# Kernel tuning notes

Hardware: AMD Instinct MI355X
Metric: run time of the kernel (lower is better)

The kernel has to match this reference:

```python
import jax, jax.numpy as jnp
import numpy as np

DIM = 1024
HID = 2816
N_ROUTED = 7  # num_experts - num_shared_experts
TOPK = 2
B, S = 4, 2048


def _expert(x, wg, wu, wd):
    # DeepSeekExpertLayer: down(silu(gate(x)) * up(x)); weights stored [in, out]
    return (jax.nn.silu(x @ wg) * (x @ wu)) @ wd


def setup_inputs() -> dict:
    key = jax.random.key(0)
    ks = jax.random.split(key, 9)
    s = 0.02
    x = jax.random.normal(ks[0], (B, S, DIM), jnp.float32)
    shared_gate = jax.random.normal(ks[1], (DIM, HID), jnp.float32) * s
    shared_up = jax.random.normal(ks[2], (DIM, HID), jnp.float32) * s
    shared_down = jax.random.normal(ks[3], (HID, DIM), jnp.float32) * s
    routed_gate = jax.random.normal(ks[4], (N_ROUTED, DIM, HID), jnp.float32) * s
    routed_up = jax.random.normal(ks[5], (N_ROUTED, DIM, HID), jnp.float32) * s
    routed_down = jax.random.normal(ks[6], (N_ROUTED, HID, DIM), jnp.float32) * s
    Wr = jax.random.normal(ks[7], (DIM, N_ROUTED), jnp.float32) * s
    # NOTE: original inits routing_bias to zeros (degenerate routing since logits
    # are MULTIPLIED by it); use random values so routing is non-trivial.
    routing_bias = jax.random.normal(ks[8], (N_ROUTED,), jnp.float32)
    return dict(x=x, shared_gate=shared_gate, shared_up=shared_up, shared_down=shared_down,
                routed_gate=routed_gate, routed_up=routed_up, routed_down=routed_down,
                Wr=Wr, routing_bias=routing_bias)


def reference(x, shared_gate, shared_up, shared_down,
              routed_gate, routed_up, routed_down, Wr, routing_bias):
    b, s, d = x.shape
    n_exp = routed_gate.shape[0]
    # shared expert path (num_shared_experts == 1, no division)
    shared_out = _expert(x, shared_gate, shared_up, shared_down)
    # router: note logits are MULTIPLIED by routing_bias (faithful to source)
    logits = (x @ Wr) * routing_bias            # [b, s, E]
    probs = jax.nn.sigmoid(logits)
    scores, idx = jax.lax.top_k(probs, TOPK)    # [b, s, k]
    scores = scores / scores.sum(-1, keepdims=True)
    # per-token per-expert combine weight via scatter-add of top-k scores
    t = b * s
    xf = x.reshape(t, d)
    weights = jnp.zeros((t, n_exp), x.dtype).at[
        jnp.arange(t)[:, None], idx.reshape(t, TOPK)].add(scores.reshape(t, TOPK))
    combined = jnp.zeros_like(xf)
    for e in range(n_exp):  # static small loop over experts
        combined = combined + _expert(xf, routed_gate[e], routed_up[e], routed_down[e]) * weights[:, e:e + 1]
    return shared_out + combined.reshape(b, s, d)
```

## Files before the change

### kernel.cpp

```cpp
#include <hip/hip_runtime.h>
#include <hip/hip_bf16.h>

#define DIM 1024
#define HID 2816
#define NEXP 7
#define TOKENS 8192
#define NT16 (DIM / 64)

#define MW3_XB    0ull
#define MW3_WGU   16777216ull
#define MW3_WD    109051904ull
#define MW3_H     155189248ull
#define MW3_TOK   303693824ull
#define MW3_WGT   303799296ull
#define MW3_SLT   303904768ull
#define MW3_META  303970304ull
#define MW3_NEED  303972352ull

#define MW_XB    0ull
#define MW_H     16777216ull
#define MW_WGU   114098176ull
#define MW_WD    206372864ull
#define MW_TOK   252510208ull
#define MW_WGT   252579328ull
#define MW_META  252648448ull
#define MW_NEED  252650496ull

typedef __bf16 bf16x8 __attribute__((ext_vector_type(8)));
typedef float f32x4 __attribute__((ext_vector_type(4)));

static __device__ __forceinline__ unsigned short f2b(float f) {
  union { float f; unsigned int i; } c; c.f = f;
  unsigned int i = c.i;
  unsigned int r = (i + 0x7fffu + ((i >> 16) & 1u)) >> 16;
  return (unsigned short)r;
}

static __device__ __forceinline__ void gload16(const void* g, void* l) {
  __builtin_amdgcn_global_load_lds(
      (const __attribute__((address_space(1))) unsigned int*)g,
      (__attribute__((address_space(3))) unsigned int*)l, 16, 0, 0);
}

__global__ __launch_bounds__(256, 2) void router_kernel(
    const float* __restrict__ X,
    const float* __restrict__ Wr,
    const float* __restrict__ bias,
    int* __restrict__ eidx,
    float* __restrict__ ew)
{
  __shared__ float wr[DIM * NEXP];
  for (int i = threadIdx.x; i < DIM * NEXP; i += 256) wr[i] = Wr[i];
  __syncthreads();
  int t = blockIdx.x * 256 + threadIdx.x;
  float acc[NEXP];
#pragma unroll
  for (int e = 0; e < NEXP; ++e) acc[e] = 0.f;
  const float* xp = X + (size_t)t * DIM;
  for (int d0 = 0; d0 < DIM; d0 += 4) {
    float4 xv = *(const float4*)(xp + d0);
    const float* xs = (const float*)&xv;
#pragma unroll
    for (int j = 0; j < 4; ++j) {
      float xf = xs[j];
#pragma unroll
      for (int e = 0; e < NEXP; ++e) acc[e] += xf * wr[(d0 + j) * NEXP + e];
    }
  }
  float p[NEXP];
#pragma unroll
  for (int e = 0; e < NEXP; ++e)
    p[e] = 1.f / (1.f + __expf(-acc[e] * bias[e]));
  float best = -1.f; int bi = 0;
#pragma unroll
  for (int e = 0; e < NEXP; ++e) if (p[e] > best) { best = p[e]; bi = e; }
  float sec = -1.f; int si = 0;
#pragma unroll
  for (int e = 0; e < NEXP; ++e) if (e != bi && p[e] > sec) { sec = p[e]; si = e; }
  float s = best + sec;
  eidx[t] = bi | (si << 8);
  ((float2*)ew)[t] = make_float2(best / s, sec / s);
}

__global__ __launch_bounds__(256) void xcvt_kernel(
    const float* __restrict__ X, unsigned short* __restrict__ Xb)
{
  int i = (blockIdx.x * 256 + threadIdx.x) * 8;
  float4 v0 = *(const float4*)&X[i];
  float4 v1 = *(const float4*)&X[i + 4];
  unsigned short o[8];
  o[0] = f2b(v0.x); o[1] = f2b(v0.y); o[2] = f2b(v0.z); o[3] = f2b(v0.w);
  o[4] = f2b(v1.x); o[5] = f2b(v1.y); o[6] = f2b(v1.z); o[7] = f2b(v1.w);
  *(int4*)&Xb[i] = *(const int4*)o;
}

__global__ __launch_bounds__(256) void build3_kernel(
    const int* __restrict__ eidx, const float* __restrict__ ew,
    int* __restrict__ tok, float* __restrict__ wgt,
    int2* __restrict__ slt, int* __restrict__ meta)
{
  __shared__ int cnt[NEXP], fill[NEXP], ofs[NEXP];
  const int tid = threadIdx.x;
  const int lane = tid & 63, wid = tid >> 6;
  if (tid < NEXP) { cnt[tid] = 0; fill[tid] = 0; }
  for (int i = tid; i < TOKENS; i += 256) { tok[i] = i; wgt[i] = 1.f; }
  __syncthreads();
  const unsigned long long lmask = (1ull << lane) - 1ull;
  for (int base = wid * 64; base < TOKENS; base += 256) {
    int t = base + lane;
    int p = eidx[t];
    int e0 = p & 0xff, e1 = (p >> 8) & 0xff;
#pragma unroll
    for (int e = 0; e < NEXP; ++e) {
      unsigned long long m0 = __ballot(e0 == e);
      unsigned long long m1 = __ballot(e1 == e);
      if (lane == 0) {
        int tot = __popcll(m0) + __popcll(m1);
        if (tot) atomicAdd(&cnt[e], tot);
      }
    }
  }
  __syncthreads();
  if (tid == 0) {
    int o = 0, nb = 0, nb2 = 0;
    meta[0] = TOKENS; meta[8] = 0;
    for (int i = 0; i < TOKENS / 256; ++i) meta[32 + nb++] = 0 | (i << 4);
    for (int i = 0; i < TOKENS / 128; ++i) meta[160 + nb2++] = 0 | (i << 4);
    for (int e = 0; e < NEXP; ++e) {
      ofs[e] = o;
      meta[1 + e] = cnt[e];
      meta[9 + e] = TOKENS + o;
      int b = (cnt[e] + 255) >> 8;
      for (int i = 0; i < b; ++i)     meta[32 + nb++]   = (e + 1) | (i << 4);
      for (int i = 0; i < 2 * b; ++i) meta[160 + nb2++] = (e + 1) | (i << 4);
      o += b << 8;
    }
    meta[16] = nb; meta[17] = nb2;
  }
  __syncthreads();
  for (int base = wid * 64; base < TOKENS; base += 256) {
    int t = base + lane;
    int p = eidx[t];
    int e0 = p & 0xff, e1 = (p >> 8) & 0xff;
    float2 w = ((const float2*)ew)[t];
    int s0 = 0, s1 = 0;
#pragma unroll
    for (int e = 0; e < NEXP; ++e) {
      unsigned long long m0 = __ballot(e0 == e);
      unsigned long long m1 = __ballot(e1 == e);
      int tot = __popcll(m0) + __popcll(m1);
      int wb = 0;
      if (lane == 0 && tot) wb = atomicAdd(&fill[e], tot);
      wb = __shfl(wb, 0);
      if (e0 == e) {
        int sl = TOKENS + ofs[e] + wb + __popcll(m0 & lmask);
        tok[sl] = t; wgt[sl] = w.x; s0 = sl;
      }
      if (e1 == e) {
        int sl = TOKENS + ofs[e] + wb + __popcll(m0) + __popcll(m1 & lmask);
        tok[sl] = t; wgt[sl] = w.y; s1 = sl;
      }
    }
    slt[t] = make_int2(s0, s1);
  }
}

__global__ __launch_bounds__(256) void transpose_all_kernel(
    const float* __restrict__ sg, const float* __restrict__ su, const float* __restrict__ sd,
    const float* __restrict__ rg, const float* __restrict__ ru, const float* __restrict__ rd,
    unsigned short* __restrict__ WguA, unsigned short* __restrict__ WdA)
{
  int b = blockIdx.x;
  int e = b / 2112, r = b % 2112;
  int m = r / 704, q2 = r % 704;
  const float* src; unsigned short* dst; int K, N, nb, kb;
  if (m == 0) {
    src = e ? rg + (size_t)(e - 1) * DIM * HID : sg;
    dst = WguA + (size_t)e * (2 * (size_t)HID * DIM);
    K = DIM; N = HID; nb = q2 % 44; kb = q2 / 44;
  } else if (m == 1) {
    src = e ? ru + (size_t)(e - 1) * DIM * HID : su;
    dst = WguA + (size_t)e * (2 * (size_t)HID * DIM) + (size_t)HID * DIM;
    K = DIM; N = HID; nb = q2 % 44; kb = q2 / 44;
  } else {
    src = e ? rd + (size_t)(e - 1) * HID * DIM : sd;
    dst = WdA + (size_t)e * ((size_t)HID * DIM);
    K = HID; N = DIM; nb = q2 % 16; kb = q2 / 16;
  }
  __shared__ unsigned short t[64][72];
  const int n0 = nb * 64, k0 = kb * 64;
  const int tid = threadIdx.x;
  const int kl = tid >> 4, nl = (tid & 15) * 4;
#pragma unroll
  for (int i = 0; i < 4; ++i) {
    int k = kl + i * 16;
    float4 v = *(const float4*)&src[(size_t)(k0 + k) * N + n0 + nl];
    t[nl + 0][k] = f2b(v.x); t[nl + 1][k] = f2b(v.y);
    t[nl + 2][k] = f2b(v.z); t[nl + 3][k] = f2b(v.w);
  }
  __syncthreads();
  const int nl2 = tid >> 3, kc = (tid & 7) * 8;
#pragma unroll
  for (int i = 0; i < 2; ++i) {
    int n = nl2 + i * 32;
    *(int4*)&dst[(size_t)(n0 + n) * K + k0 + kc] = *(const int4*)&t[n][kc];
  }
}

__global__ __launch_bounds__(512, 2) void gateup8_kernel(
    const unsigned short* __restrict__ Xb,
    const unsigned short* __restrict__ WguA,
    const int* __restrict__ tok, const float* __restrict__ wgt,
    const int* __restrict__ meta,
    unsigned short* __restrict__ H)
{
  const int yb = blockIdx.y;
  if (yb >= meta[16]) return;
  const int ent = meta[32 + yb];
  const int e = ent & 15, mb = ent >> 4;
  const int cnt = meta[e];
  const int pofs = meta[8 + e];
  const int m0 = mb * 256;
  const unsigned short* Wg = WguA + (size_t)e * (2 * (size_t)HID * DIM);
  const unsigned short* Wu = Wg + (size_t)HID * DIM;

  __shared__ __align__(16) unsigned short As[3][256 * 64];
  __shared__ __align__(16) unsigned short Bgs[3][64 * 64];
  __shared__ __align__(16) unsigned short Bus[3][64 * 64];
  __shared__ float wl[256];

  const int tid = threadIdx.x;
  const int lane = tid & 63;
  const int w = tid >> 6;
  const int wmi = w & 3;
  const int wni = w >> 2;
  const int c = lane & 15;
  const int q = lane >> 4;
  const int cx = c & 7;

  const int srow = tid >> 3;
  const int swz = ((tid & 7) ^ (srow & 7)) * 8;

  const unsigned short* aptr[4];
#pragma unroll
  for (int i = 0; i < 4; ++i) {
    int s = m0 + i * 64 + srow;
    int t = (s < cnt) ? tok[pofs + s] : 0;
    aptr[i] = Xb + (size_t)t * DIM + swz;
  }
  const int n0 = blockIdx.x * 64;
  const unsigned short* gptr = Wg + (size_t)(n0 + srow) * DIM + swz;
  const unsigned short* uptr = Wu + (size_t)(n0 + srow) * DIM + swz;

  if (tid < 256) wl[tid] = (m0 + tid < cnt) ? wgt[pofs + m0 + tid] : 0.f;

#pragma unroll
  for (int t = 0; t < 2; ++t) {
#pragma unroll
    for (int i = 0; i < 4; ++i) gload16(aptr[i] + t * 64, &As[t][i * 4096 + tid * 8]);
    gload16(gptr + t * 64, &Bgs[t][tid * 8]);
    gload16(uptr + t * 64, &Bus[t][tid * 8]);
  }
  __syncthreads();

  f32x4 accg[4][2], accu[4][2];
#pragma unroll
  for (int mi = 0; mi < 4; ++mi)
#pragma unroll
    for (int ni = 0; ni < 2; ++ni) {
      accg[mi][ni] = {0.f, 0.f, 0.f, 0.f};
      accu[mi][ni] = {0.f, 0.f, 0.f, 0.f};
    }

  int b = 0, bs = 2;
#pragma unroll 1
  for (int t = 0; t < NT16; ++t) {
    bf16x8 a[4][2], bg[2][2];
#pragma unroll
    for (int mi = 0; mi < 4; ++mi)
#pragma unroll
      for (int ks = 0; ks < 2; ++ks)
        a[mi][ks] = *(const bf16x8*)&As[b][(wmi * 64 + mi * 16 + c) * 64 + (((ks * 4 + q) ^ cx) * 8)];
#pragma unroll
    for (int ni = 0; ni < 2; ++ni)
#pragma unroll
      for (int ks = 0; ks < 2; ++ks)
        bg[ni][ks] = *(const bf16x8*)&Bgs[b][(wni * 32 + ni * 16 + c) * 64 + (((ks * 4 + q) ^ cx) * 8)];
    if (t + 2 < NT16) {
      const int k2 = (t + 2) * 64;
      gload16(aptr[0] + k2, &As[bs][0 * 4096 + tid * 8]);
      gload16(aptr[1] + k2, &As[bs][1 * 4096 + tid * 8]);
      gload16(aptr[2] + k2, &As[bs][2 * 4096 + tid * 8]);
    }
    __builtin_amdgcn_s_barrier();
    asm volatile("s_waitcnt lgkmcnt(0)" ::: "memory");
    __builtin_amdgcn_sched_barrier(0);
    __builtin_amdgcn_s_setprio(1);
#pragma unroll
    for (int mi = 0; mi < 4; ++mi)
#pragma unroll
      for (int ni = 0; ni < 2; ++ni) {
        accg[mi][ni] = __builtin_amdgcn_mfma_f32_16x16x32_bf16(a[mi][0], bg[ni][0], accg[mi][ni], 0, 0, 0);
        accg[mi][ni] = __builtin_amdgcn_mfma_f32_16x16x32_bf16(a[mi][1], bg[ni][1], accg[mi][ni], 0, 0, 0);
      }
    __builtin_amdgcn_s_setprio(0);
    __builtin_amdgcn_sched_barrier(0);
    __builtin_amdgcn_s_barrier();
    __builtin_amdgcn_sched_barrier(0);

    bf16x8 bu[2][2];
#pragma unroll
    for (int ni = 0; ni < 2; ++ni)
#pragma unroll
      for (int ks = 0; ks < 2; ++ks)
        bu[ni][ks] = *(const bf16x8*)&Bus[b][(wni * 32 + ni * 16 + c) * 64 + (((ks * 4 + q) ^ cx) * 8)];
    if (t + 2 < NT16) {
      const int k2 = (t + 2) * 64;
      gload16(aptr[3] + k2, &As[bs][3 * 4096 + tid * 8]);
      gload16(gptr + k2, &Bgs[bs][tid * 8]);
      gload16(uptr + k2, &Bus[bs][tid * 8]);
      asm volatile("s_waitcnt vmcnt(6)" ::: "memory");
    } else if (t + 1 < NT16) {
      asm volatile("s_waitcnt vmcnt(0)" ::: "memory");
    }
    __builtin_amdgcn_s_barrier();
    asm volatile("s_waitcnt lgkmcnt(0)" ::: "memory");
    __builtin_amdgcn_sched_barrier(0);
    __builtin_amdgcn_s_setprio(1);
#pragma unroll
    for (int mi = 0; mi < 4; ++mi)
#pragma unroll
      for (int ni = 0; ni < 2; ++ni) {
        accu[mi][ni] = __builtin_amdgcn_mfma_f32_16x16x32_bf16(a[mi][0], bu[ni][0], accu[mi][ni], 0, 0, 0);
        accu[mi][ni] = __builtin_amdgcn_mfma_f32_16x16x32_bf16(a[mi][1], bu[ni][1], accu[mi][ni], 0, 0, 0);
      }
    __builtin_amdgcn_s_setprio(0);
    __builtin_amdgcn_sched_barrier(0);
    __builtin_amdgcn_s_barrier();
    __builtin_amdgcn_sched_barrier(0);

    b = (b == 2) ? 0 : b + 1;
    bs = (bs == 2) ? 0 : bs + 1;
  }

#pragma unroll
  for (int mi = 0; mi < 4; ++mi)
#pragma unroll
    for (int ni = 0; ni < 2; ++ni)
#pragma unroll
      for (int r = 0; r < 4; ++r) {
        int row = wmi * 64 + mi * 16 + q * 4 + r;
        int col = wni * 32 + ni * 16 + c;
        float g = accg[mi][ni][r];
        float u = accu[mi][ni][r];
        float h = (g / (1.f + __expf(-g))) * u * wl[row];
        H[(size_t)(pofs + m0 + row) * HID + n0 + col] = f2b(h);
      }
}

__global__ __launch_bounds__(256, 2) void down_all_kernel(
    const unsigned short* __restrict__ Hm,
    const unsigned short* __restrict__ WdA,
    const int* __restrict__ meta,
    float* __restrict__ P)
{
  const int yb = blockIdx.y;
  if (yb >= meta[17]) return;
  const int ent = meta[160 + yb];
  const int e = ent & 15, mb = ent >> 4;
  const int pofs = meta[8 + e];
  const unsigned short* WdT = WdA + (size_t)e * ((size_t)HID * DIM);

  __shared__ __align__(16) unsigned short As[128 * 64];
  __shared__ __align__(16) unsigned short Bs[128 * 64];
  const int n0 = blockIdx.x * 128;
  const int tid = threadIdx.x;
  const int lane = tid & 63;
  const int w4 = tid >> 6;
  const int wm = (w4 & 1) * 64;
  const int wn = (w4 >> 1) * 64;
  const int c = lane & 15;
  const int q = lane >> 4;
  const int cx = c & 7;

  const int r8 = lane >> 3;
  const int swz = ((lane & 7) ^ r8) * 8;
  const int wrow = w4 * 8 + r8;

  const unsigned short* aptr[4];
  const unsigned short* bptr[4];
#pragma unroll
  for (int i = 0; i < 4; ++i) {
    aptr[i] = Hm + (size_t)(pofs + mb * 128 + i * 32 + wrow) * HID + swz;
    bptr[i] = WdT + (size_t)(n0 + i * 32 + wrow) * HID + swz;
  }

  f32x4 acc[4][4];
#pragma unroll
  for (int mi = 0; mi < 4; ++mi)
#pragma unroll
    for (int ni = 0; ni < 4; ++ni) acc[mi][ni] = {0.f, 0.f, 0.f, 0.f};

  for (int k0 = 0; k0 < HID; k0 += 64) {
    __syncthreads();
#pragma unroll
    for (int i = 0; i < 4; ++i) {
      gload16(aptr[i] + k0, &As[i * 2048 + tid * 8]);
      gload16(bptr[i] + k0, &Bs[i * 2048 + tid * 8]);
    }
    __syncthreads();
#pragma unroll
    for (int h = 0; h < 2; ++h) {
      const int go = ((h * 4 + q) ^ cx) * 8;
      bf16x8 a[4], bb[4];
#pragma unroll
      for (int mi = 0; mi < 4; ++mi)
        a[mi] = *(const bf16x8*)&As[(wm + mi * 16 + c) * 64 + go];
#pragma unroll
      for (int ni = 0; ni < 4; ++ni)
        bb[ni] = *(const bf16x8*)&Bs[(wn + ni * 16 + c) * 64 + go];
#pragma unroll
      for (int mi = 0; mi < 4; ++mi)
#pragma unroll
        for (int ni = 0; ni < 4; ++ni)
          acc[mi][ni] = __builtin_amdgcn_mfma_f32_16x16x32_bf16(a[mi], bb[ni], acc[mi][ni], 0, 0, 0);
    }
  }
#pragma unroll
  for (int mi = 0; mi < 4; ++mi)
#pragma unroll
    for (int r = 0; r < 4; ++r) {
      int prow = pofs + mb * 128 + wm + mi * 16 + q * 4 + r;
#pragma unroll
      for (int ni = 0; ni < 4; ++ni) {
        int col = n0 + wn + ni * 16 + c;
        P[(size_t)prow * DIM + col] = acc[mi][ni][r];
      }
    }
}

__global__ __launch_bounds__(256) void combine_kernel(
    const float* __restrict__ P, const int2* __restrict__ slt,
    float* __restrict__ out)
{
  const int t = blockIdx.x;
  const int2 s = slt[t];
  const int d = threadIdx.x;
  float4 a = ((const float4*)(P + (size_t)t * DIM))[d];
  float4 b = ((const float4*)(P + (size_t)s.x * DIM))[d];
  float4 cc = ((const float4*)(P + (size_t)s.y * DIM))[d];
  float4 o;
  o.x = a.x + b.x + cc.x; o.y = a.y + b.y + cc.y;
  o.z = a.z + b.z + cc.z; o.w = a.w + b.w + cc.w;
  ((float4*)(out + (size_t)t * DIM))[d] = o;
}

__global__ __launch_bounds__(256) void build_kernel(
    const int* __restrict__ eidx, const float* __restrict__ ew,
    int* __restrict__ tok, float* __restrict__ wgt, int* __restrict__ meta,
    int padmode)
{
  __shared__ int cnt[NEXP], fill[NEXP], ofs[NEXP];
  if (threadIdx.x < NEXP) { cnt[threadIdx.x] = 0; fill[threadIdx.x] = 0; }
  __syncthreads();
  for (int t = threadIdx.x; t < TOKENS; t += 256) {
    int p = eidx[t];
    atomicAdd(&cnt[p & 0xff], 1);
    atomicAdd(&cnt[(p >> 8) & 0xff], 1);
  }
  __syncthreads();
  if (threadIdx.x == 0) {
    int o = 0, nb = 0;
    for (int e = 0; e < NEXP; ++e) {
      ofs[e] = o;
      meta[e] = cnt[e];
      meta[8 + e] = o;
      if (padmode) {
        int b = (cnt[e] + 127) >> 7;
        for (int i = 0; i < b; ++i) meta[16 + nb++] = e | (i << 3);
        o += b << 7;
      } else {
        o += cnt[e];
      }
    }
    meta[15] = nb;
  }
  __syncthreads();
  for (int t = threadIdx.x; t < TOKENS; t += 256) {
    int p = eidx[t];
    int e0 = p & 0xff, e1 = (p >> 8) & 0xff;
    float2 w = ((const float2*)ew)[t];
    int p0 = ofs[e0] + atomicAdd(&fill[e0], 1);
    tok[p0] = t; wgt[p0] = w.x;
    int p1 = ofs[e1] + atomicAdd(&fill[e1], 1);
    tok[p1] = t; wgt[p1] = w.y;
  }
}

__global__ __launch_bounds__(256, 2) void gateup_kernel(
    const unsigned short* __restrict__ Xb,
    const unsigned short* __restrict__ Wgu,
    unsigned short* __restrict__ H)
{
  __shared__ __align__(16) unsigned short As[128 * 64];
  __shared__ __align__(16) unsigned short Bgs[64 * 64];
  __shared__ __align__(16) unsigned short Bus[64 * 64];
  const int m0 = blockIdx.y * 128;
  const int n0 = blockIdx.x * 64;
  const int tid = threadIdx.x;
  const int lane = tid & 63;
  const int w = tid >> 6;
  const int wm = (w & 1) * 64;
  const int wn = (w >> 1) * 32;
  const int c = lane & 15;
  const int q = lane >> 4;
  const int cx = c & 7;
  const unsigned short* Wg = Wgu;
  const unsigned short* Wu = Wgu + (size_t)HID * DIM;
  const int r8 = lane >> 3;
  const int swz = ((lane & 7) ^ r8) * 8;
  const int wrow = w * 8 + r8;
  const unsigned short* aptr[4];
#pragma unroll
  for (int i = 0; i < 4; ++i)
    aptr[i] = Xb + (size_t)(m0 + i * 32 + wrow) * DIM + swz;
  const unsigned short* gptr[2];
  const unsigned short* uptr[2];
#pragma unroll
  for (int i = 0; i < 2; ++i) {
    gptr[i] = Wg + (size_t)(n0 + i * 32 + wrow) * DIM + swz;
    uptr[i] = Wu + (size_t)(n0 + i * 32 + wrow) * DIM + swz;
  }
  f32x4 accg[4][2], accu[4][2];
#pragma unroll
  for (int mi = 0; mi < 4; ++mi)
#pragma unroll
    for (int ni = 0; ni < 2; ++ni) {
      accg[mi][ni] = {0.f, 0.f, 0.f, 0.f};
      accu[mi][ni] = {0.f, 0.f, 0.f, 0.f};
    }
  for (int k0 = 0; k0 < DIM; k0 += 64) {
    __syncthreads();
#pragma unroll
    for (int i = 0; i < 4; ++i) gload16(aptr[i] + k0, &As[i * 2048 + tid * 8]);
#pragma unroll
    for (int i = 0; i < 2; ++i) {
      gload16(gptr[i] + k0, &Bgs[i * 2048 + tid * 8]);
      gload16(uptr[i] + k0, &Bus[i * 2048 + tid * 8]);
    }
    __syncthreads();
#pragma unroll
    for (int h = 0; h < 2; ++h) {
      const int go = ((h * 4 + q) ^ cx) * 8;
      bf16x8 a[4], bg[2], bu[2];
#pragma unroll
      for (int mi = 0; mi < 4; ++mi)
        a[mi] = *(const bf16x8*)&As[(wm + mi * 16 + c) * 64 + go];
#pragma unroll
      for (int ni = 0; ni < 2; ++ni) {
        bg[ni] = *(const bf16x8*)&Bgs[(wn + ni * 16 + c) * 64 + go];
        bu[ni] = *(const bf16x8*)&Bus[(wn + ni * 16 + c) * 64 + go];
      }
#pragma unroll
      for (int mi = 0; mi < 4; ++mi)
#pragma unroll
        for (int ni = 0; ni < 2; ++ni) {
          accg[mi][ni] = __builtin_amdgcn_mfma_f32_16x16x32_bf16(a[mi], bg[ni], accg[mi][ni], 0, 0, 0);
          accu[mi][ni] = __builtin_amdgcn_mfma_f32_16x16x32_bf16(a[mi], bu[ni], accu[mi][ni], 0, 0, 0);
        }
    }
  }
#pragma unroll
  for (int mi = 0; mi < 4; ++mi)
#pragma unroll
    for (int ni = 0; ni < 2; ++ni)
#pragma unroll
      for (int r = 0; r < 4; ++r) {
        int row = wm + mi * 16 + q * 4 + r;
        int col = wn + ni * 16 + c;
        float g = accg[mi][ni][r];
        float u = accu[mi][ni][r];
        float h = (g / (1.f + __expf(-g))) * u;
        H[(size_t)(m0 + row) * HID + n0 + col] = f2b(h);
      }
}

__global__ __launch_bounds__(256, 2) void gateup_sparse_all_kernel(
    const unsigned short* __restrict__ Xb,
    const unsigned short* __restrict__ WguR,
    const int* __restrict__ tok, const float* __restrict__ wgt,
    const int* __restrict__ meta,
    unsigned short* __restrict__ H)
{
  const int yb = blockIdx.y;
  if (yb >= meta[15]) return;
  const int bm = meta[16 + yb];
  const int e = bm & 7, mb = bm >> 3;
  const int cnt = meta[e];
  const int pofs = meta[8 + e];
  const unsigned short* Wgu = WguR + (size_t)e * (2 * (size_t)HID * DIM);
  __shared__ __align__(16) unsigned short As[128 * 64];
  __shared__ __align__(16) unsigned short Bgs[64 * 64];
  __shared__ __align__(16) unsigned short Bus[64 * 64];
  __shared__ float wl[128];
  const int n0 = blockIdx.x * 64;
  const int tid = threadIdx.x;
  const int lane = tid & 63;
  const int w = tid >> 6;
  const int wm = (w & 1) * 64;
  const int wn = (w >> 1) * 32;
  const int c = lane & 15;
  const int q = lane >> 4;
  const int cx = c & 7;
  if (tid < 128)
    wl[tid] = (mb * 128 + tid < cnt) ? wgt[pofs + mb * 128 + tid] : 0.f;
  const unsigned short* Wg = Wgu;
  const unsigned short* Wu = Wgu + (size_t)HID * DIM;
  const int r8 = lane >> 3;
  const int swz = ((lane & 7) ^ r8) * 8;
  const int wrow = w * 8 + r8;
  const unsigned short* aptr[4];
#pragma unroll
  for (int i = 0; i < 4; ++i) {
    int s = mb * 128 + i * 32 + wrow;
    int t = (s < cnt) ? tok[pofs + s] : 0;
    aptr[i] = Xb + (size_t)t * DIM + swz;
  }
  const unsigned short* gptr[2];
  const unsigned short* uptr[2];
#pragma unroll
  for (int i = 0; i < 2; ++i) {
    gptr[i] = Wg + (size_t)(n0 + i * 32 + wrow) * DIM + swz;
    uptr[i] = Wu + (size_t)(n0 + i * 32 + wrow) * DIM + swz;
  }
  f32x4 accg[4][2], accu[4][2];
#pragma unroll
  for (int mi = 0; mi < 4; ++mi)
#pragma unroll
    for (int ni = 0; ni < 2; ++ni) {
      accg[mi][ni] = {0.f, 0.f, 0.f, 0.f};
      accu[mi][ni] = {0.f, 0.f, 0.f, 0.f};
    }
  for (int k0 = 0; k0 < DIM; k0 += 64) {
    __syncthreads();
#pragma unroll
    for (int i = 0; i < 4; ++i) gload16(aptr[i] + k0, &As[i * 2048 + tid * 8]);
#pragma unroll
    for (int i = 0; i < 2; ++i) {
      gload16(gptr[i] + k0, &Bgs[i * 2048 + tid * 8]);
      gload16(uptr[i] + k0, &Bus[i * 2048 + tid * 8]);
    }
    __syncthreads();
#pragma unroll
    for (int h = 0; h < 2; ++h) {
      const int go = ((h * 4 + q) ^ cx) * 8;
      bf16x8 a[4], bg[2], bu[2];
#pragma unroll
      for (int mi = 0; mi < 4; ++mi)
        a[mi] = *(const bf16x8*)&As[(wm + mi * 16 + c) * 64 + go];
#pragma unroll
      for (int ni = 0; ni < 2; ++ni) {
        bg[ni] = *(const bf16x8*)&Bgs[(wn + ni * 16 + c) * 64 + go];
        bu[ni] = *(const bf16x8*)&Bus[(wn + ni * 16 + c) * 64 + go];
      }
#pragma unroll
      for (int mi = 0; mi < 4; ++mi)
#pragma unroll
        for (int ni = 0; ni < 2; ++ni) {
          accg[mi][ni] = __builtin_amdgcn_mfma_f32_16x16x32_bf16(a[mi], bg[ni], accg[mi][ni], 0, 0, 0);
          accu[mi][ni] = __builtin_amdgcn_mfma_f32_16x16x32_bf16(a[mi], bu[ni], accu[mi][ni], 0, 0, 0);
        }
    }
  }
#pragma unroll
  for (int mi = 0; mi < 4; ++mi)
#pragma unroll
    for (int ni = 0; ni < 2; ++ni)
#pragma unroll
      for (int r = 0; r < 4; ++r) {
        int row = wm + mi * 16 + q * 4 + r;
        int col = wn + ni * 16 + c;
        float g = accg[mi][ni][r];
        float u = accu[mi][ni][r];
        float h = (g / (1.f + __expf(-g))) * u * wl[row];
        H[(size_t)(pofs + mb * 128 + row) * HID + n0 + col] = f2b(h);
      }
}

__global__ __launch_bounds__(256, 2) void down_dense_kernel(
    const unsigned short* __restrict__ Hm,
    const unsigned short* __restrict__ WdT,
    float* __restrict__ out)
{
  __shared__ __align__(16) unsigned short As[128 * 64];
  __shared__ __align__(16) unsigned short Bs[128 * 64];
  const int m0 = blockIdx.y * 128;
  const int n0 = blockIdx.x * 128;
  const int tid = threadIdx.x;
  const int lane = tid & 63;
  const int w4 = tid >> 6;
  const int wm = (w4 & 1) * 64;
  const int wn = (w4 >> 1) * 64;
  const int c = lane & 15;
  const int q = lane >> 4;
  const int cx = c & 7;
  const int r8 = lane >> 3;
  const int swz = ((lane & 7) ^ r8) * 8;
  const int wrow = w4 * 8 + r8;
  const unsigned short* aptr[4];
  const unsigned short* bptr[4];
#pragma unroll
  for (int i = 0; i < 4; ++i) {
    aptr[i] = Hm + (size_t)(m0 + i * 32 + wrow) * HID + swz;
    bptr[i] = WdT + (size_t)(n0 + i * 32 + wrow) * HID + swz;
  }
  f32x4 acc[4][4];
#pragma unroll
  for (int mi = 0; mi < 4; ++mi)
#pragma unroll
    for (int ni = 0; ni < 4; ++ni) acc[mi][ni] = {0.f, 0.f, 0.f, 0.f};
  for (int k0 = 0; k0 < HID; k0 += 64) {
    __syncthreads();
#pragma unroll
    for (int i = 0; i < 4; ++i) {
      gload16(aptr[i] + k0, &As[i * 2048 + tid * 8]);
      gload16(bptr[i] + k0, &Bs[i * 2048 + tid * 8]);
    }
    __syncthreads();
#pragma unroll
    for (int h = 0; h < 2; ++h) {
      const int go = ((h * 4 + q) ^ cx) * 8;
      bf16x8 a[4], bb[4];
#pragma unroll
      for (int mi = 0; mi < 4; ++mi)
        a[mi] = *(const bf16x8*)&As[(wm + mi * 16 + c) * 64 + go];
#pragma unroll
      for (int ni = 0; ni < 4; ++ni)
        bb[ni] = *(const bf16x8*)&Bs[(wn + ni * 16 + c) * 64 + go];
#pragma unroll
      for (int mi = 0; mi < 4; ++mi)
#pragma unroll
        for (int ni = 0; ni < 4; ++ni)
          acc[mi][ni] = __builtin_amdgcn_mfma_f32_16x16x32_bf16(a[mi], bb[ni], acc[mi][ni], 0, 0, 0);
    }
  }
#pragma unroll
  for (int mi = 0; mi < 4; ++mi)
#pragma unroll
    for (int r = 0; r < 4; ++r) {
      int trow = m0 + wm + mi * 16 + q * 4 + r;
#pragma unroll
      for (int ni = 0; ni < 4; ++ni) {
        int col = n0 + wn + ni * 16 + c;
        out[(size_t)trow * DIM + col] = acc[mi][ni][r];
      }
    }
}

__global__ __launch_bounds__(256, 2) void down_sparse_all_kernel(
    const unsigned short* __restrict__ Hm,
    const unsigned short* __restrict__ WdR,
    const int* __restrict__ tok, const int* __restrict__ meta,
    float* __restrict__ out)
{
  const int yb = blockIdx.y;
  if (yb >= meta[15]) return;
  const int bm = meta[16 + yb];
  const int e = bm & 7, mb = bm >> 3;
  const int cnt = meta[e];
  const int pofs = meta[8 + e];
  const unsigned short* WdT = WdR + (size_t)e * ((size_t)HID * DIM);
  const int kbase = blockIdx.z * (HID / 2);
  __shared__ __align__(16) unsigned short As[128 * 64];
  __shared__ __align__(16) unsigned short Bs[128 * 64];
  __shared__ int tl[128];
  const int n0 = blockIdx.x * 128;
  const int tid = threadIdx.x;
  const int lane = tid & 63;
  const int w4 = tid >> 6;
  const int wm = (w4 & 1) * 64;
  const int wn = (w4 >> 1) * 64;
  const int c = lane & 15;
  const int q = lane >> 4;
  const int cx = c & 7;
  if (tid < 128)
    tl[tid] = (mb * 128 + tid < cnt) ? tok[pofs + mb * 128 + tid] : 0;
  const int r8 = lane >> 3;
  const int swz = ((lane & 7) ^ r8) * 8;
  const int wrow = w4 * 8 + r8;
  const unsigned short* aptr[4];
  const unsigned short* bptr[4];
#pragma unroll
  for (int i = 0; i < 4; ++i) {
    aptr[i] = Hm + (size_t)(mb * 128 + i * 32 + wrow) * HID + kbase + swz;
    bptr[i] = WdT + (size_t)(n0 + i * 32 + wrow) * HID + kbase + swz;
  }
  f32x4 acc[4][4];
#pragma unroll
  for (int mi = 0; mi < 4; ++mi)
#pragma unroll
    for (int ni = 0; ni < 4; ++ni) acc[mi][ni] = {0.f, 0.f, 0.f, 0.f};
  for (int k0 = 0; k0 < HID / 2; k0 += 64) {
    __syncthreads();
#pragma unroll
    for (int i = 0; i < 4; ++i) {
      gload16(aptr[i] + k0, &As[i * 2048 + tid * 8]);
      gload16(bptr[i] + k0, &Bs[i * 2048 + tid * 8]);
    }
    __syncthreads();
#pragma unroll
    for (int h = 0; h < 2; ++h) {
      const int go = ((h * 4 + q) ^ cx) * 8;
      bf16x8 a[4], bb[4];
#pragma unroll
      for (int mi = 0; mi < 4; ++mi)
        a[mi] = *(const bf16x8*)&As[(wm + mi * 16 + c) * 64 + go];
#pragma unroll
      for (int ni = 0; ni < 4; ++ni)
        bb[ni] = *(const bf16x8*)&Bs[(wn + ni * 16 + c) * 64 + go];
#pragma unroll
      for (int mi = 0; mi < 4; ++mi)
#pragma unroll
        for (int ni = 0; ni < 4; ++ni)
          acc[mi][ni] = __builtin_amdgcn_mfma_f32_16x16x32_bf16(a[mi], bb[ni], acc[mi][ni], 0, 0, 0);
    }
  }
#pragma unroll
  for (int mi = 0; mi < 4; ++mi)
#pragma unroll
    for (int r = 0; r < 4; ++r) {
      int lr = wm + mi * 16 + q * 4 + r;
      if (mb * 128 + lr < cnt) {
        int t = tl[lr];
#pragma unroll
        for (int ni = 0; ni < 4; ++ni) {
          int col = n0 + wn + ni * 16 + c;
          atomicAdd(&out[(size_t)t * DIM + col], acc[mi][ni][r]);
        }
      }
    }
}

extern "C" void kernel_launch(void* const* d_in, const int* in_sizes, int n_in,
                              void* d_out, int out_size, void* d_ws, size_t ws_size,
                              hipStream_t stream) {
  (void)in_sizes; (void)n_in; (void)out_size;
  const float* x   = (const float*)d_in[0];
  const float* sg  = (const float*)d_in[1];
  const float* su  = (const float*)d_in[2];
  const float* sd  = (const float*)d_in[3];
  const float* rg  = (const float*)d_in[4];
  const float* ru  = (const float*)d_in[5];
  const float* rd  = (const float*)d_in[6];
  const float* wrr = (const float*)d_in[7];
  const float* rb  = (const float*)d_in[8];
  float* out = (float*)d_out;

  char* ws = (char*)d_ws;
  dim3 blk(256);

  if (ws_size >= MW3_NEED) {
    unsigned short* Xb   = (unsigned short*)(ws + MW3_XB);
    unsigned short* WguA = (unsigned short*)(ws + MW3_WGU);
    unsigned short* WdA  = (unsigned short*)(ws + MW3_WD);
    unsigned short* H    = (unsigned short*)(ws + MW3_H);
    int*   tok           = (int*)(ws + MW3_TOK);
    float* wgt           = (float*)(ws + MW3_WGT);
    int2*  slt           = (int2*)(ws + MW3_SLT);
    int*   meta          = (int*)(ws + MW3_META);
    float* P             = (float*)ws;
    int*   eidx = (int*)H;
    float* ew   = (float*)((char*)H + 32768);

    router_kernel<<<dim3(TOKENS / 256), blk, 0, stream>>>(x, wrr, rb, eidx, ew);
    xcvt_kernel<<<dim3(TOKENS * DIM / (8 * 256)), blk, 0, stream>>>(x, Xb);
    build3_kernel<<<dim3(1), blk, 0, stream>>>(eidx, ew, tok, wgt, slt, meta);
    transpose_all_kernel<<<dim3(8 * 2112), blk, 0, stream>>>(sg, su, sd, rg, ru, rd, WguA, WdA);
    gateup8_kernel<<<dim3(HID / 64, 104), dim3(512), 0, stream>>>(Xb, WguA, tok, wgt, meta, H);
    down_all_kernel<<<dim3(DIM / 128, 208), blk, 0, stream>>>(H, WdA, meta, P);
    combine_kernel<<<dim3(TOKENS), blk, 0, stream>>>(P, slt, out);
  } else {
    unsigned short* Xb   = (unsigned short*)(ws + MW_XB);
    unsigned short* H    = (unsigned short*)(ws + MW_H);
    unsigned short* WguA = (unsigned short*)(ws + MW_WGU);
    unsigned short* WdA  = (unsigned short*)(ws + MW_WD);
    int*   tok           = (int*)(ws + MW_TOK);
    float* wgt           = (float*)(ws + MW_WGT);
    int*   meta          = (int*)(ws + MW_META);
    int*   eidx = (int*)H;
    float* ew   = (float*)((char*)H + 32768);

    router_kernel<<<dim3(TOKENS / 256), blk, 0, stream>>>(x, wrr, rb, eidx, ew);
    xcvt_kernel<<<dim3(TOKENS * DIM / (8 * 256)), blk, 0, stream>>>(x, Xb);
    build_kernel<<<dim3(1), blk, 0, stream>>>(eidx, ew, tok, wgt, meta, 1);
    transpose_all_kernel<<<dim3(8 * 2112), blk, 0, stream>>>(sg, su, sd, rg, ru, rd, WguA, WdA);
    gateup_kernel<<<dim3(HID / 64, TOKENS / 128), blk, 0, stream>>>(Xb, WguA, H);
    down_dense_kernel<<<dim3(DIM / 128, TOKENS / 128), blk, 0, stream>>>(H, WdA, out);
    const unsigned short* WguRt = WguA + 2 * (size_t)HID * DIM;
    const unsigned short* WdRt  = WdA + (size_t)HID * DIM;
    gateup_sparse_all_kernel<<<dim3(HID / 64, 135), blk, 0, stream>>>(Xb, WguRt, tok, wgt, meta, H);
    down_sparse_all_kernel<<<dim3(DIM / 128, 135, 2), blk, 0, stream>>>(H, WdRt, tok, meta, out);
  }
}
```

Before: 1.036 ms.

## Fuse routed combine into split-K down GEMM with atomics; simplify gate/up loop

Drops the per-slot partial buffer P and the separate combine kernel. A dense down GEMM now writes the shared-expert output directly, then a split-K routed down kernel atomically adds each token's weighted expert contribution into the output. The gate/up kernel's hand-tuned triple-buffered pipeline with barriers and priorities is replaced by a simple single-buffer load-sync-compute loop, and H is written with nontemporal stores. This saves one kernel and the P round-trip, but adds float atomics and non-deterministic summation order, and gives up load/compute overlap in the largest GEMM.

Result: faster. 999.1 us (-3.6%).

```diff
diff --git a/kernel.cpp b/kernel.cpp
--- a/kernel.cpp
+++ b/kernel.cpp
@@ -5,7 +5,6 @@
 #define HID 2816
 #define NEXP 7
 #define TOKENS 8192
-#define NT16 (DIM / 64)
 
 #define MW3_XB    0ull
 #define MW3_WGU   16777216ull
@@ -94,10 +93,9 @@
   *(int4*)&Xb[i] = *(const int4*)o;
 }
 
-__global__ __launch_bounds__(256) void build3_kernel(
+__global__ __launch_bounds__(256) void build4_kernel(
     const int* __restrict__ eidx, const float* __restrict__ ew,
-    int* __restrict__ tok, float* __restrict__ wgt,
-    int2* __restrict__ slt, int* __restrict__ meta)
+    int* __restrict__ tok, float* __restrict__ wgt, int* __restrict__ meta)
 {
   __shared__ int cnt[NEXP], fill[NEXP], ofs[NEXP];
   const int tid = threadIdx.x;
@@ -125,7 +123,6 @@
     int o = 0, nb = 0, nb2 = 0;
     meta[0] = TOKENS; meta[8] = 0;
     for (int i = 0; i < TOKENS / 256; ++i) meta[32 + nb++] = 0 | (i << 4);
-    for (int i = 0; i < TOKENS / 128; ++i) meta[160 + nb2++] = 0 | (i << 4);
     for (int e = 0; e < NEXP; ++e) {
       ofs[e] = o;
       meta[1 + e] = cnt[e];
@@ -143,7 +140,6 @@
     int p = eidx[t];
     int e0 = p & 0xff, e1 = (p >> 8) & 0xff;
     float2 w = ((const float2*)ew)[t];
-    int s0 = 0, s1 = 0;
 #pragma unroll
     for (int e = 0; e < NEXP; ++e) {
       unsigned long long m0 = __ballot(e0 == e);
@@ -154,14 +150,13 @@
       wb = __shfl(wb, 0);
       if (e0 == e) {
         int sl = TOKENS + ofs[e] + wb + __popcll(m0 & lmask);
-        tok[sl] = t; wgt[sl] = w.x; s0 = sl;
+        tok[sl] = t; wgt[sl] = w.x;
       }
       if (e1 == e) {
         int sl = TOKENS + ofs[e] + wb + __popcll(m0) + __popcll(m1 & lmask);
-        tok[sl] = t; wgt[sl] = w.y; s1 = sl;
-      }
-    }
-    slt[t] = make_int2(s0, s1);
+        tok[sl] = t; wgt[sl] = w.y;
+      }
+    }
   }
 }
 
@@ -207,7 +202,7 @@
   }
 }
 
-__global__ __launch_bounds__(512, 2) void gateup8_kernel(
+__global__ __launch_bounds__(512, 2) void gateup_all256_kernel(
     const unsigned short* __restrict__ Xb,
     const unsigned short* __restrict__ WguA,
     const int* __restrict__ tok, const float* __restrict__ wgt,
@@ -224,9 +219,9 @@
   const unsigned short* Wg = WguA + (size_t)e * (2 * (size_t)HID * DIM);
   const unsigned short* Wu = Wg + (size_t)HID * DIM;
 
-  __shared__ __align__(16) unsigned short As[3][256 * 64];
-  __shared__ __align__(16) unsigned short Bgs[3][64 * 64];
-  __shared__ __align__(16) unsigned short Bus[3][64 * 64];
+  __shared__ __align__(16) unsigned short As[256 * 64];
+  __shared__ __align__(16) unsigned short Bgs[64 * 64];
+  __shared__ __align__(16) unsigned short Bus[64 * 64];
   __shared__ float wl[256];
 
   const int tid = threadIdx.x;
@@ -254,15 +249,6 @@
 
   if (tid < 256) wl[tid] = (m0 + tid < cnt) ? wgt[pofs + m0 + tid] : 0.f;
 
-#pragma unroll
-  for (int t = 0; t < 2; ++t) {
-#pragma unroll
-    for (int i = 0; i < 4; ++i) gload16(aptr[i] + t * 64, &As[t][i * 4096 + tid * 8]);
-    gload16(gptr + t * 64, &Bgs[t][tid * 8]);
-    gload16(uptr + t * 64, &Bus[t][tid * 8]);
-  }
-  __syncthreads();
-
   f32x4 accg[4][2], accu[4][2];
 #pragma unroll
   for (int mi = 0; mi < 4; ++mi)
@@ -272,77 +258,34 @@
       accu[mi][ni] = {0.f, 0.f, 0.f, 0.f};
     }
 
-  int b = 0, bs = 2;
-#pragma unroll 1
-  for (int t = 0; t < NT16; ++t) {
-    bf16x8 a[4][2], bg[2][2];
-#pragma unroll
-    for (int mi = 0; mi < 4; ++mi)
-#pragma unroll
-      for (int ks = 0; ks < 2; ++ks)
-        a[mi][ks] = *(const bf16x8*)&As[b][(wmi * 64 + mi * 16 + c) * 64 + (((ks * 4 + q) ^ cx) * 8)];
-#pragma unroll
-    for (int ni = 0; ni < 2; ++ni)
-#pragma unroll
-      for (int ks = 0; ks < 2; ++ks)
-        bg[ni][ks] = *(const bf16x8*)&Bgs[b][(wni * 32 + ni * 16 + c) * 64 + (((ks * 4 + q) ^ cx) * 8)];
-    if (t + 2 < NT16) {
-      const int k2 = (t + 2) * 64;
-      gload16(aptr[0] + k2, &As[bs][0 * 4096 + tid * 8]);
-      gload16(aptr[1] + k2, &As[bs][1 * 4096 + tid * 8]);
-      gload16(aptr[2] + k2, &As[bs][2 * 4096 + tid * 8]);
-    }
-    __builtin_amdgcn_s_barrier();
-    asm volatile("s_waitcnt lgkmcnt(0)" ::: "memory");
-    __builtin_amdgcn_sched_barrier(0);
-    __builtin_amdgcn_s_setprio(1);
-#pragma unroll
-    for (int mi = 0; mi < 4; ++mi)
+  for (int k0 = 0; k0 < DIM; k0 += 64) {
+    __syncthreads();
+#pragma unroll
+    for (int i = 0; i < 4; ++i) gload16(aptr[i] + k0, &As[i * 4096 + tid * 8]);
+    gload16(gptr + k0, &Bgs[tid * 8]);
+    gload16(uptr + k0, &Bus[tid * 8]);
+    __syncthreads();
+#pragma unroll
+    for (int h = 0; h < 2; ++h) {
+      const int go = ((h * 4 + q) ^ cx) * 8;
+      bf16x8 a[4], bg[2], bu[2];
+#pragma unroll
+      for (int mi = 0; mi < 4; ++mi)
+        a[mi] = *(const bf16x8*)&As[(wmi * 64 + mi * 16 + c) * 64 + go];
 #pragma unroll
       for (int ni = 0; ni < 2; ++ni) {
-        accg[mi][ni] = __builtin_amdgcn_mfma_f32_16x16x32_bf16(a[mi][0], bg[ni][0], accg[mi][ni], 0, 0, 0);
-        accg[mi][ni] = __builtin_amdgcn_mfma_f32_16x16x32_bf16(a[mi][1], bg[ni][1], accg[mi][ni], 0, 0, 0);
-      }
-    __builtin_amdgcn_s_setprio(0);
-    __builtin_amdgcn_sched_barrier(0);
-    __builtin_amdgcn_s_barrier();
-    __builtin_amdgcn_sched_barrier(0);
-
-    bf16x8 bu[2][2];
-#pragma unroll
-    for (int ni = 0; ni < 2; ++ni)
-#pragma unroll
-      for (int ks = 0; ks < 2; ++ks)
-        bu[ni][ks] = *(const bf16x8*)&Bus[b][(wni * 32 + ni * 16 + c) * 64 + (((ks * 4 + q) ^ cx) * 8)];
-    if (t + 2 < NT16) {
-      const int k2 = (t + 2) * 64;
-      gload16(aptr[3] + k2, &As[bs][3 * 4096 + tid * 8]);
-      gload16(gptr + k2, &Bgs[bs][tid * 8]);
-      gload16(uptr + k2, &Bus[bs][tid * 8]);
-      asm volatile("s_waitcnt vmcnt(6)" ::: "memory");
-    } else if (t + 1 < NT16) {
-      asm volatile("s_waitcnt vmcnt(0)" ::: "memory");
-    }
-    __builtin_amdgcn_s_barrier();
-    asm volatile("s_waitcnt lgkmcnt(0)" ::: "memory");
-    __builtin_amdgcn_sched_barrier(0);
-    __builtin_amdgcn_s_setprio(1);
-#pragma unroll
-    for (int mi = 0; mi < 4; ++mi)
-#pragma unroll
-      for (int ni = 0; ni < 2; ++ni) {
-        accu[mi][ni] = __builtin_amdgcn_mfma_f32_16x16x32_bf16(a[mi][0], bu[ni][0], accu[mi][ni], 0, 0, 0);
-        accu[mi][ni] = __builtin_amdgcn_mfma_f32_16x16x32_bf16(a[mi][1], bu[ni][1], accu[mi][ni], 0, 0, 0);
-      }
-    __builtin_amdgcn_s_setprio(0);
-    __builtin_amdgcn_sched_barrier(0);
-    __builtin_amdgcn_s_barrier();
-    __builtin_amdgcn_sched_barrier(0);
-
-    b = (b == 2) ? 0 : b + 1;
-    bs = (bs == 2) ? 0 : bs + 1;
-  }
-
+        bg[ni] = *(const bf16x8*)&Bgs[(wni * 32 + ni * 16 + c) * 64 + go];
+        bu[ni] = *(const bf16x8*)&Bus[(wni * 32 + ni * 16 + c) * 64 + go];
+      }
+#pragma unroll
+      for (int mi = 0; mi < 4; ++mi)
+#pragma unroll
+        for (int ni = 0; ni < 2; ++ni) {
+          accg[mi][ni] = __builtin_amdgcn_mfma_f32_16x16x32_bf16(a[mi], bg[ni], accg[mi][ni], 0, 0, 0);
+          accu[mi][ni] = __builtin_amdgcn_mfma_f32_16x16x32_bf16(a[mi], bu[ni], accu[mi][ni], 0, 0, 0);
+        }
+    }
+  }
 #pragma unroll
   for (int mi = 0; mi < 4; ++mi)
 #pragma unroll
@@ -354,25 +297,19 @@
         float g = accg[mi][ni][r];
         float u = accu[mi][ni][r];
         float h = (g / (1.f + __expf(-g))) * u * wl[row];
-        H[(size_t)(pofs + m0 + row) * HID + n0 + col] = f2b(h);
-      }
-}
-
-__global__ __launch_bounds__(256, 2) void down_all_kernel(
+        unsigned short hv = f2b(h);
+        __builtin_nontemporal_store(hv, &H[(size_t)(pofs + m0 + row) * HID + n0 + col]);
+      }
+}
+
+__global__ __launch_bounds__(256, 2) void down_dense_kernel(
     const unsigned short* __restrict__ Hm,
-    const unsigned short* __restrict__ WdA,
-    const int* __restrict__ meta,
-    float* __restrict__ P)
-{
-  const int yb = blockIdx.y;
-  if (yb >= meta[17]) return;
-  const int ent = meta[160 + yb];
-  const int e = ent & 15, mb = ent >> 4;
-  const int pofs = meta[8 + e];
-  const unsigned short* WdT = WdA + (size_t)e * ((size_t)HID * DIM);
-
+    const unsigned short* __restrict__ WdT,
+    float* __restrict__ out)
+{
   __shared__ __align__(16) unsigned short As[128 * 64];
   __shared__ __align__(16) unsigned short Bs[128 * 64];
+  const int m0 = blockIdx.y * 128;
   const int n0 = blockIdx.x * 128;
   const int tid = threadIdx.x;
   const int lane = tid & 63;
@@ -382,25 +319,21 @@
   const int c = lane & 15;
   const int q = lane >> 4;
   const int cx = c & 7;
-
   const int r8 = lane >> 3;
   const int swz = ((lane & 7) ^ r8) * 8;
   const int wrow = w4 * 8 + r8;
-
   const unsigned short* aptr[4];
   const unsigned short* bptr[4];
 #pragma unroll
   for (int i = 0; i < 4; ++i) {
-    aptr[i] = Hm + (size_t)(pofs + mb * 128 + i * 32 + wrow) * HID + swz;
+    aptr[i] = Hm + (size_t)(m0 + i * 32 + wrow) * HID + swz;
     bptr[i] = WdT + (size_t)(n0 + i * 32 + wrow) * HID + swz;
   }
-
   f32x4 acc[4][4];
 #pragma unroll
   for (int mi = 0; mi < 4; ++mi)
 #pragma unroll
     for (int ni = 0; ni < 4; ++ni) acc[mi][ni] = {0.f, 0.f, 0.f, 0.f};
-
   for (int k0 = 0; k0 < HID; k0 += 64) {
     __syncthreads();
 #pragma unroll
@@ -430,29 +363,98 @@
   for (int mi = 0; mi < 4; ++mi)
 #pragma unroll
     for (int r = 0; r < 4; ++r) {
-      int prow = pofs + mb * 128 + wm + mi * 16 + q * 4 + r;
+      int trow = m0 + wm + mi * 16 + q * 4 + r;
 #pragma unroll
       for (int ni = 0; ni < 4; ++ni) {
         int col = n0 + wn + ni * 16 + c;
-        P[(size_t)prow * DIM + col] = acc[mi][ni][r];
-      }
-    }
-}
-
-__global__ __launch_bounds__(256) void combine_kernel(
-    const float* __restrict__ P, const int2* __restrict__ slt,
+        out[(size_t)trow * DIM + col] = acc[mi][ni][r];
+      }
+    }
+}
+
+__global__ __launch_bounds__(256, 2) void down_routed_kernel(
+    const unsigned short* __restrict__ Hm,
+    const unsigned short* __restrict__ WdA,
+    const int* __restrict__ tok, const int* __restrict__ meta,
     float* __restrict__ out)
 {
-  const int t = blockIdx.x;
-  const int2 s = slt[t];
-  const int d = threadIdx.x;
-  float4 a = ((const float4*)(P + (size_t)t * DIM))[d];
-  float4 b = ((const float4*)(P + (size_t)s.x * DIM))[d];
-  float4 cc = ((const float4*)(P + (size_t)s.y * DIM))[d];
-  float4 o;
-  o.x = a.x + b.x + cc.x; o.y = a.y + b.y + cc.y;
-  o.z = a.z + b.z + cc.z; o.w = a.w + b.w + cc.w;
-  ((float4*)(out + (size_t)t * DIM))[d] = o;
+  const int yb = blockIdx.y;
+  if (yb >= meta[17]) return;
+  const int ent = meta[160 + yb];
+  const int e = ent & 15, mb = ent >> 4;
+  const int cnt = meta[e];
+  const int pofs = meta[8 + e];
+  const unsigned short* WdT = WdA + (size_t)e * ((size_t)HID * DIM);
+  const int kbase = blockIdx.z * (HID / 2);
+
+  __shared__ __align__(16) unsigned short As[128 * 64];
+  __shared__ __align__(16) unsigned short Bs[128 * 64];
+  __shared__ int tl[128];
+  const int n0 = blockIdx.x * 128;
+  const int tid = threadIdx.x;
+  const int lane = tid & 63;
+  const int w4 = tid >> 6;
+  const int wm = (w4 & 1) * 64;
+  const int wn = (w4 >> 1) * 64;
+  const int c = lane & 15;
+  const int q = lane >> 4;
+  const int cx = c & 7;
+  if (tid < 128)
+    tl[tid] = (mb * 128 + tid < cnt) ? tok[pofs + mb * 128 + tid] : 0;
+  const int r8 = lane >> 3;
+  const int swz = ((lane & 7) ^ r8) * 8;
+  const int wrow = w4 * 8 + r8;
+  const unsigned short* aptr[4];
+  const unsigned short* bptr[4];
+#pragma unroll
+  for (int i = 0; i < 4; ++i) {
+    aptr[i] = Hm + (size_t)(pofs + mb * 128 + i * 32 + wrow) * HID + kbase + swz;
+    bptr[i] = WdT + (size_t)(n0 + i * 32 + wrow) * HID + kbase + swz;
+  }
+  f32x4 acc[4][4];
+#pragma unroll
+  for (int mi = 0; mi < 4; ++mi)
+#pragma unroll
+    for (int ni = 0; ni < 4; ++ni) acc[mi][ni] = {0.f, 0.f, 0.f, 0.f};
+  for (int k0 = 0; k0 < HID / 2; k0 += 64) {
+    __syncthreads();
+#pragma unroll
+    for (int i = 0; i < 4; ++i) {
+      gload16(aptr[i] + k0, &As[i * 2048 + tid * 8]);
+      gload16(bptr[i] + k0, &Bs[i * 2048 + tid * 8]);
+    }
+    __syncthreads();
+#pragma unroll
+    for (int h = 0; h < 2; ++h) {
+      const int go = ((h * 4 + q) ^ cx) * 8;
+      bf16x8 a[4], bb[4];
+#pragma unroll
+      for (int mi = 0; mi < 4; ++mi)
+        a[mi] = *(const bf16x8*)&As[(wm + mi * 16 + c) * 64 + go];
+#pragma unroll
+      for (int ni = 0; ni < 4; ++ni)
+        bb[ni] = *(const bf16x8*)&Bs[(wn + ni * 16 + c) * 64 + go];
+#pragma unroll
+      for (int mi = 0; mi < 4; ++mi)
+#pragma unroll
+        for (int ni = 0; ni < 4; ++ni)
+          acc[mi][ni] = __builtin_amdgcn_mfma_f32_16x16x32_bf16(a[mi], bb[ni], acc[mi][ni], 0, 0, 0);
+    }
+  }
+#pragma unroll
+  for (int mi = 0; mi < 4; ++mi)
+#pragma unroll
+    for (int r = 0; r < 4; ++r) {
+      int lr = wm + mi * 16 + q * 4 + r;
+      if (mb * 128 + lr < cnt) {
+        int t = tl[lr];
+#pragma unroll
+        for (int ni = 0; ni < 4; ++ni) {
+          int col = n0 + wn + ni * 16 + c;
+          atomicAdd(&out[(size_t)t * DIM + col], acc[mi][ni][r]);
+        }
+      }
+    }
 }
 
 __global__ __launch_bounds__(256) void build_kernel(
@@ -687,76 +689,6 @@
       }
 }
 
-__global__ __launch_bounds__(256, 2) void down_dense_kernel(
-    const unsigned short* __restrict__ Hm,
-    const unsigned short* __restrict__ WdT,
-    float* __restrict__ out)
-{
-  __shared__ __align__(16) unsigned short As[128 * 64];
-  __shared__ __align__(16) unsigned short Bs[128 * 64];
-  const int m0 = blockIdx.y * 128;
-  const int n0 = blockIdx.x * 128;
-  const int tid = threadIdx.x;
-  const int lane = tid & 63;
-  const int w4 = tid >> 6;
-  const int wm = (w4 & 1) * 64;
-  const int wn = (w4 >> 1) * 64;
-  const int c = lane & 15;
-  const int q = lane >> 4;
-  const int cx = c & 7;
-  const int r8 = lane >> 3;
-  const int swz = ((lane & 7) ^ r8) * 8;
-  const int wrow = w4 * 8 + r8;
-  const unsigned short* aptr[4];
-  const unsigned short* bptr[4];
-#pragma unroll
-  for (int i = 0; i < 4; ++i) {
-    aptr[i] = Hm + (size_t)(m0 + i * 32 + wrow) * HID + swz;
-    bptr[i] = WdT + (size_t)(n0 + i * 32 + wrow) * HID + swz;
-  }
-  f32x4 acc[4][4];
-#pragma unroll
-  for (int mi = 0; mi < 4; ++mi)
-#pragma unroll
-    for (int ni = 0; ni < 4; ++ni) acc[mi][ni] = {0.f, 0.f, 0.f, 0.f};
-  for (int k0 = 0; k0 < HID; k0 += 64) {
-    __syncthreads();
-#pragma unroll
-    for (int i = 0; i < 4; ++i) {
-      gload16(aptr[i] + k0, &As[i * 2048 + tid * 8]);
-      gload16(bptr[i] + k0, &Bs[i * 2048 + tid * 8]);
-    }
-    __syncthreads();
-#pragma unroll
-    for (int h = 0; h < 2; ++h) {
-      const int go = ((h * 4 + q) ^ cx) * 8;
-      bf16x8 a[4], bb[4];
-#pragma unroll
-      for (int mi = 0; mi < 4; ++mi)
-        a[mi] = *(const bf16x8*)&As[(wm + mi * 16 + c) * 64 + go];
-#pragma unroll
-      for (int ni = 0; ni < 4; ++ni)
-        bb[ni] = *(const bf16x8*)&Bs[(wn + ni * 16 + c) * 64 + go];
-#pragma unroll
-      for (int mi = 0; mi < 4; ++mi)
-#pragma unroll
-        for (int ni = 0; ni < 4; ++ni)
-          acc[mi][ni] = __builtin_amdgcn_mfma_f32_16x16x32_bf16(a[mi], bb[ni], acc[mi][ni], 0, 0, 0);
-    }
-  }
-#pragma unroll
-  for (int mi = 0; mi < 4; ++mi)
-#pragma unroll
-    for (int r = 0; r < 4; ++r) {
-      int trow = m0 + wm + mi * 16 + q * 4 + r;
-#pragma unroll
-      for (int ni = 0; ni < 4; ++ni) {
-        int col = n0 + wn + ni * 16 + c;
-        out[(size_t)trow * DIM + col] = acc[mi][ni][r];
-      }
-    }
-}
-
 __global__ __launch_bounds__(256, 2) void down_sparse_all_kernel(
     const unsigned short* __restrict__ Hm,
     const unsigned short* __restrict__ WdR,
@@ -792,7 +724,7 @@
   const unsigned short* bptr[4];
 #pragma unroll
   for (int i = 0; i < 4; ++i) {
-    aptr[i] = Hm + (size_t)(mb * 128 + i * 32 + wrow) * HID + kbase + swz;
+    aptr[i] = Hm + (size_t)(pofs + mb * 128 + i * 32 + wrow) * HID + kbase + swz;
     bptr[i] = WdT + (size_t)(n0 + i * 32 + wrow) * HID + kbase + swz;
   }
   f32x4 acc[4][4];
@@ -866,19 +798,17 @@
     unsigned short* H    = (unsigned short*)(ws + MW3_H);
     int*   tok           = (int*)(ws + MW3_TOK);
     float* wgt           = (float*)(ws + MW3_WGT);
-    int2*  slt           = (int2*)(ws + MW3_SLT);
     int*   meta          = (int*)(ws + MW3_META);
-    float* P             = (float*)ws;
     int*   eidx = (int*)H;
     float* ew   = (float*)((char*)H + 32768);
 
     router_kernel<<<dim3(TOKENS / 256), blk, 0, stream>>>(x, wrr, rb, eidx, ew);
     xcvt_kernel<<<dim3(TOKENS * DIM / (8 * 256)), blk, 0, stream>>>(x, Xb);
-    build3_kernel<<<dim3(1), blk, 0, stream>>>(eidx, ew, tok, wgt, slt, meta);
+    build4_kernel<<<dim3(1), blk, 0, stream>>>(eidx, ew, tok, wgt, meta);
     transpose_all_kernel<<<dim3(8 * 2112), blk, 0, stream>>>(sg, su, sd, rg, ru, rd, WguA, WdA);
-    gateup8_kernel<<<dim3(HID / 64, 104), dim3(512), 0, stream>>>(Xb, WguA, tok, wgt, meta, H);
-    down_all_kernel<<<dim3(DIM / 128, 208), blk, 0, stream>>>(H, WdA, meta, P);
-    combine_kernel<<<dim3(TOKENS), blk, 0, stream>>>(P, slt, out);
+    gateup_all256_kernel<<<dim3(HID / 64, 104), dim3(512), 0, stream>>>(Xb, WguA, tok, wgt, meta, H);
+    down_dense_kernel<<<dim3(DIM / 128, TOKENS / 128), blk, 0, stream>>>(H, WdA, out);
+    down_routed_kernel<<<dim3(DIM / 128, 144, 2), blk, 0, stream>>>(H, WdA, tok, meta, out);
   } else {
     unsigned short* Xb   = (unsigned short*)(ws + MW_XB);
     unsigned short* H    = (unsigned short*)(ws + MW_H);
```
